# Performance work log

Hardware: AMD Instinct MI355X
Metric: run time of the kernel (lower is better)

The kernel has to match this reference:

```python
import jax, jax.numpy as jnp
import numpy as np

N_PROP, N_GRID, N_KEY, C_FEAT = 128, 216, 4096, 128
RADII = (0.8, 1.6)
NSAMPLES = (16, 16)
C_OUT = 64  # per-branch MLP output channels


def setup_inputs() -> dict:
    key = jax.random.key(0)
    ks = jax.random.split(key, 20)
    s = 0.05
    return {
        "wlh": jax.random.uniform(ks[0], (N_PROP, 3)) * 4.0 + 0.5,
        "center": jax.random.normal(ks[1], (N_PROP, 3)) * 5.0,
        "yaw": jax.random.uniform(ks[2], (N_PROP,)) * 2.0 * np.pi,
        "u": jax.random.uniform(ks[3], (N_PROP, N_GRID, 3)),
        "keypoints_xyz": jax.random.normal(ks[4], (1, N_KEY, 3)) * 5.0,
        "keypoints_features": jax.random.normal(ks[5], (1, C_FEAT, N_KEY)),
        "pn0_w1": jax.random.normal(ks[6], (C_OUT, C_FEAT + 3)) * s,
        "pn0_g1": jnp.ones((C_OUT,)), "pn0_b1": jnp.zeros((C_OUT,)),
        "pn0_w2": jax.random.normal(ks[7], (C_OUT, C_OUT)) * s,
        "pn0_g2": jnp.ones((C_OUT,)), "pn0_b2": jnp.zeros((C_OUT,)),
        "pn1_w1": jax.random.normal(ks[8], (C_OUT, C_FEAT + 3)) * s,
        "pn1_g1": jnp.ones((C_OUT,)), "pn1_b1": jnp.zeros((C_OUT,)),
        "pn1_w2": jax.random.normal(ks[9], (C_OUT, C_OUT)) * s,
        "pn1_g2": jnp.ones((C_OUT,)), "pn1_b2": jnp.zeros((C_OUT,)),
        "red_w1": jax.random.normal(ks[10], (256, N_GRID * 2 * C_OUT)) * 0.01,
        "red_b1": jnp.zeros((256,)),
        "red_w2": jax.random.normal(ks[11], (256, 256)) * s,
        "red_b2": jnp.zeros((256,)),
    }


def reference(wlh, center, yaw, u, keypoints_xyz, keypoints_features,
              pn0_w1, pn0_g1, pn0_b1, pn0_w2, pn0_g2, pn0_b2,
              pn1_w1, pn1_g1, pn1_b1, pn1_w2, pn1_g2, pn1_b2,
              red_w1, red_b1, red_w2, red_b2):
    n, m, _ = u.shape
    # --- sample gridpoints inside proposals and rotate by yaw around z ---
    gp = u * wlh[:, None, :]                                 # (n, m, 3)
    c, s = jnp.cos(yaw), jnp.sin(yaw)
    R = jnp.stack([c, -s, s, c], axis=-1).reshape(-1, 2, 2)   # (n, 2, 2)
    xy = jnp.einsum('njk,nmk->nmj', R, gp[..., :2])
    grid = jnp.concatenate([xy, gp[..., 2:]], -1) + center[:, None, :]
    grid = grid.reshape(-1, 3)                               # (G, 3), G = n*m

    kp = keypoints_xyz[0]                                    # (K, 3)
    kf = jnp.transpose(keypoints_features[0])                # (K, C)
    K = kp.shape[0]

    # squared distances (G, K) without materializing (G, K, 3)
    d2 = (jnp.sum(grid * grid, -1)[:, None]
          + jnp.sum(kp * kp, -1)[None, :]
          - 2.0 * grid @ kp.T)

    def ball_query(radius, nsample):
        # first `nsample` in-radius indices in original order; pad with first
        # hit; all-zeros if no point in radius (pointnet2 CUDA semantics).
        mask = d2 < radius * radius
        cand = jnp.where(mask, jnp.arange(K, dtype=jnp.int32), K)
        srt = jnp.sort(cand, axis=-1)[:, :nsample]           # (G, ns)
        first = srt[:, :1]
        return jnp.where(srt < K, srt, jnp.where(first < K, first, 0))

    def branch(radius, nsample, w1, g1, b1, w2, g2, b2):
        idx = ball_query(radius, nsample)                    # (G, ns)
        xyz = kp[idx] - grid[:, None, :]                     # (G, ns, 3)
        x = jnp.concatenate([xyz, kf[idx]], -1)              # (G, ns, 3+C)
        h = jax.nn.relu(jnp.einsum('gnc,oc->gno', x, w1) * g1 + b1)
        h = jax.nn.relu(jnp.einsum('gnc,oc->gno', h, w2) * g2 + b2)
        return jnp.max(h, axis=1)                            # (G, C_OUT)

    f0 = branch(RADII[0], NSAMPLES[0], pn0_w1, pn0_g1, pn0_b1, pn0_w2, pn0_g2, pn0_b2)
    f1 = branch(RADII[1], NSAMPLES[1], pn1_w1, pn1_g1, pn1_b1, pn1_w2, pn1_g2, pn1_b2)
    pooled = jnp.concatenate([f0, f1], -1)                   # (G, 2*C_OUT)
    Cp = pooled.shape[-1]

    # faithful replication of (1,C,n,m).permute(0,3,1,2).view(1,n,-1)
    t = pooled.reshape(n, m, Cp)                             # gridpoint order (n, m)
    red_in = jnp.transpose(t, (1, 2, 0)).reshape(1, n, m * Cp)

    h = jax.nn.relu(red_in @ red_w1.T + red_b1)
    return jax.nn.relu(h @ red_w2.T + red_b2)                # (1, n, 256)
```

## Files before the change

### kernel.cpp

```cpp
#include <hip/hip_runtime.h>
#include <hip/hip_bf16.h>

typedef unsigned short u16;
typedef unsigned int   u32;
typedef unsigned long long u64;

#define N_PROPC 128
#define N_GRIDC 216
#define G_TOT   27648
#define N_KEYC  4096
#define C_FEATC 128
#define R0SQ    0.64f
#define R1SQ    2.56f
#define BF16_ONES_DWORD 0x3F803F80u

typedef __attribute__((ext_vector_type(8))) short bf16x8;
typedef __attribute__((ext_vector_type(4))) float f32x4;

#if __has_builtin(__builtin_amdgcn_fcmpf)
#define BALLOT_LT(a, b) __builtin_amdgcn_fcmpf((a), (b), 4)
#else
#define BALLOT_LT(a, b) __ballot((a) < (b))
#endif

__device__ __forceinline__ float bf2f(u16 u) {
    return __uint_as_float(((u32)u) << 16);
}
__device__ __forceinline__ u16 f2bf(float f) {
    u32 u = __float_as_uint(f);
    u32 r = (u + 0x7fffu + ((u >> 16) & 1u)) >> 16;
    return (u16)r;
}
__device__ __forceinline__ bool is_bf16(const u32* flagp) {
    return *flagp == BF16_ONES_DWORD;
}
__device__ __forceinline__ float ld(const void* p, int i, bool bf) {
    return bf ? bf2f(((const u16*)p)[i]) : ((const float*)p)[i];
}
__device__ __forceinline__ u16 ldb(const void* p, int i, bool bf) {
    return bf ? ((const u16*)p)[i] : f2bf(((const float*)p)[i]);
}

__global__ __launch_bounds__(256) void prep_fused_kernel(
    const u32* __restrict__ flagp,
    const void* __restrict__ kxyz,
    const void* __restrict__ wlh, const void* __restrict__ center,
    const void* __restrict__ yaw, const void* __restrict__ uu,
    const void* __restrict__ kf,
    const void* __restrict__ w10, const void* __restrict__ g10, const void* __restrict__ b10,
    const void* __restrict__ w20, const void* __restrict__ g20, const void* __restrict__ b20,
    const void* __restrict__ w11, const void* __restrict__ g11, const void* __restrict__ b11,
    const void* __restrict__ w21, const void* __restrict__ g21, const void* __restrict__ b21,
    const void* __restrict__ rw2, const void* __restrict__ rw1,
    float4* __restrict__ kp4, float4* __restrict__ grid4, u16* __restrict__ kfT,
    u16* __restrict__ w1mf, u16* __restrict__ w2mf,
    float* __restrict__ g1f, float* __restrict__ b1f,
    float* __restrict__ g2f, float* __restrict__ b2f,
    float* __restrict__ w2rT, u16* __restrict__ rw1p)
{
    const bool bf = is_bf16(flagp);
    const int bid = blockIdx.x, tid = threadIdx.x;

    if (bid < 16) {
        int k = bid * 256 + tid;
        float x = ld(kxyz, k*3, bf), y = ld(kxyz, k*3+1, bf), z = ld(kxyz, k*3+2, bf);
        kp4[k] = make_float4(x, y, z, 0.0f);
    } else if (bid < 124) {
        int g = (bid - 16) * 256 + tid;
        int n = g / N_GRIDC;
        float ux = ld(uu, g*3, bf), uy = ld(uu, g*3+1, bf), uz = ld(uu, g*3+2, bf);
        float gpx = ux * ld(wlh, n*3, bf);
        float gpy = uy * ld(wlh, n*3+1, bf);
        float gpz = uz * ld(wlh, n*3+2, bf);
        float yv = ld(yaw, n, bf);
        float c = cosf(yv), sn = sinf(yv);
        float x = (c*gpx - sn*gpy) + ld(center, n*3, bf);
        float y = (sn*gpx + c*gpy) + ld(center, n*3+1, bf);
        float z = gpz + ld(center, n*3+2, bf);
        grid4[g] = make_float4(x, y, z, 0.0f);
    } else if (bid < 2172) {
        int t = (bid - 124) * 256 + tid;
        int key = t >> 7, feat = t & 127;
        kfT[t] = ldb(kf, feat * N_KEYC + key, bf);
    } else if (bid < 2174) {
        const int b = bid - 2172;
        const void* w1 = b ? w11 : w10; const void* g1v = b ? g11 : g10;
        const void* w2 = b ? w21 : w20; const void* g2v = b ? g21 : g20;
        const void* b1v = b ? b11 : b10; const void* b2v = b ? b21 : b20;
        for (int f = tid; f < 10240; f += 256) {
            int j = f & 7, t1 = f >> 3;
            int n = t1 & 15, t2 = t1 >> 4;
            int quad = t2 & 3, t3 = t2 >> 2;
            int kt = t3 % 5, nt = t3 / 5;
            int k = kt*32 + quad*8 + j;
            int o = nt*16 + n;
            u16 v = 0;
            if (k < 128)      v = ldb(w1, o*131 + 3 + k, bf);
            else if (k < 131) v = ldb(w1, o*131 + (k - 128), bf);
            w1mf[b*10240 + f] = v;
        }
        for (int f = tid; f < 4096; f += 256) {
            int j = f & 7, t1 = f >> 3;
            int n = t1 & 15, t2 = t1 >> 4;
            int quad = t2 & 3, t3 = t2 >> 2;
            int kt = t3 & 1, nt = t3 >> 1;
            int k = kt*32 + quad*8 + j;
            int o = nt*16 + n;
            w2mf[b*4096 + f] = ldb(w2, o*64 + k, bf);
        }
        if (tid < 64) {
            g1f[b*64 + tid] = ld(g1v, tid, bf);
            b1f[b*64 + tid] = ld(b1v, tid, bf);
            g2f[b*64 + tid] = ld(g2v, tid, bf);
            b2f[b*64 + tid] = ld(b2v, tid, bf);
        }
    } else if (bid < 2430) {
        int t = (bid - 2174) * 256 + tid;
        int o = t & 255, c = t >> 8;
        w2rT[c*256 + o] = ld(rw2, o*256 + c, bf);
    } else {
        int t = (bid - 2430) * 256 + tid;
        int j = t & 7;
        int n = (t >> 3) & 15;
        int quad = (t >> 7) & 3;
        int rest = t >> 9;
        int kk = rest % 864;
        int nt = rest / 864;
        int o = nt*16 + n;
        int k = kk*32 + quad*8 + j;
        rw1p[t] = ldb(rw1, o*27648 + k, bf);
    }
}

__global__ __launch_bounds__(256) void ballquery_kernel(
    const float4* __restrict__ kp4,
    const float4* __restrict__ grid4, u16* __restrict__ idx01)
{
    __shared__ __attribute__((aligned(16))) float4 sk[2048];
    const int tid = threadIdx.x;
    const int lane = tid & 63;
    const int g = blockIdx.x * 4 + (tid >> 6);
    const float4 gr = grid4[g];

    u64 mask0 = 0, mask1 = 0;
    #pragma unroll 1
    for (int pass = 0; pass < 2; ++pass) {
        if (pass) __syncthreads();
        for (int t = tid; t < 2048; t += 256) sk[t] = kp4[pass*2048 + t];
        __syncthreads();
        #pragma unroll
        for (int it = 0; it < 32; ++it) {
            const float4 kv = sk[it*64 + lane];
            const float dx = kv.x - gr.x;
            const float dy = kv.y - gr.y;
            const float dz = kv.z - gr.z;
            const float d = fmaf(dx, dx, fmaf(dy, dy, dz * dz));
            const u64 m1 = BALLOT_LT(d, R1SQ);
            const u64 m0 = BALLOT_LT(d, R0SQ);
            const int chunk = pass*32 + it;
            if (lane == chunk) { mask1 = m1; mask0 = m0; }
        }
    }

    u16* o0 = idx01 + (size_t)g * 16;
    u16* o1 = idx01 + (size_t)G_TOT * 16 + (size_t)g * 16;

    #pragma unroll
    for (int rad = 0; rad < 2; ++rad) {
        u64 mask = rad ? mask1 : mask0;
        u16* op = rad ? o1 : o0;
        const int cnt = __popcll(mask);
        int inc = cnt;
        #pragma unroll
        for (int d = 1; d < 64; d <<= 1) {
            int t = __shfl_up(inc, d);
            if (lane >= d) inc += t;
        }
        const int pre = inc - cnt;
        int firstk = (cnt > 0 && pre == 0) ? (lane*64 + __ffsll(mask) - 1) : 0x7FFFFFFF;
        #pragma unroll
        for (int d = 32; d >= 1; d >>= 1)
            firstk = min(firstk, __shfl_xor(firstk, d));
        const int total = __shfl(inc, 63);
        u64 mrem = mask;
        int p = pre;
        while (mrem != 0 && p < 16) {
            int j = __ffsll(mrem) - 1;
            op[p] = (u16)(lane*64 + j);
            mrem &= mrem - 1;
            ++p;
        }
        if (lane < 16 && lane >= total)
            op[lane] = (u16)(firstk == 0x7FFFFFFF ? 0 : firstk);
    }
}

__global__ __launch_bounds__(256) void pointnet_mfma_kernel(
    const float4* __restrict__ grid4, const float4* __restrict__ kp4,
    const u16* __restrict__ kfT,
    const u16* __restrict__ w1mf, const u16* __restrict__ w2mf,
    const float* __restrict__ g1f, const float* __restrict__ b1f,
    const float* __restrict__ g2f, const float* __restrict__ b2f,
    const u16* __restrict__ idx01, u16* __restrict__ ATb)
{
    __shared__ __attribute__((aligned(16))) u16 w1s[10240];
    __shared__ __attribute__((aligned(16))) u16 w2s[4096];
    __shared__ __attribute__((aligned(16))) u16 h1s[4][16*72];
    const int tid = threadIdx.x;
    const int branch = blockIdx.y;

    {
        const uint4* s1 = (const uint4*)(w1mf + branch*10240);
        uint4* d1 = (uint4*)w1s;
        for (int t = tid; t < 1280; t += 256) d1[t] = s1[t];
        const uint4* s2 = (const uint4*)(w2mf + branch*4096);
        uint4* d2 = (uint4*)w2s;
        for (int t = tid; t < 512; t += 256) d2[t] = s2[t];
    }
    __syncthreads();

    const int wid = tid >> 6, lane = tid & 63;
    const int n = lane & 15, quad = lane >> 4;
    const int g = blockIdx.x * 4 + wid;

    const int idx = idx01[(size_t)branch*(G_TOT*16) + g*16 + n] & (N_KEYC - 1);
    const float4 kp = kp4[idx];
    const float4 gr = grid4[g];

    bf16x8 axyz = (bf16x8)(short)0;
    if (quad == 0) {
        axyz[0] = (short)f2bf(kp.x - gr.x);
        axyz[1] = (short)f2bf(kp.y - gr.y);
        axyz[2] = (short)f2bf(kp.z - gr.z);
    }

    float g1v[4], b1v[4], g2v[4], b2v[4];
    #pragma unroll
    for (int nt = 0; nt < 4; ++nt) {
        g1v[nt] = g1f[branch*64 + nt*16 + n];
        b1v[nt] = b1f[branch*64 + nt*16 + n];
        g2v[nt] = g2f[branch*64 + nt*16 + n];
        b2v[nt] = b2f[branch*64 + nt*16 + n];
    }

    f32x4 acc0 = {0.f,0.f,0.f,0.f}, acc1 = acc0, acc2_ = acc0, acc3 = acc0;
    f32x4* acc[4] = {&acc0, &acc1, &acc2_, &acc3};

    const u16* __restrict__ arow = kfT + idx * C_FEATC;
    #pragma unroll
    for (int kt = 0; kt < 4; ++kt) {
        uint4 araw = *(const uint4*)(arow + kt*32 + quad*8);
        bf16x8 a;
        __builtin_memcpy(&a, &araw, 16);
        #pragma unroll
        for (int nt = 0; nt < 4; ++nt) {
            bf16x8 b = *(const bf16x8*)&w1s[(((nt*5 + kt)*4 + quad)*16 + n)*8];
            *acc[nt] = __builtin_amdgcn_mfma_f32_16x16x32_bf16(a, b, *acc[nt], 0, 0, 0);
        }
    }
    #pragma unroll
    for (int nt = 0; nt < 4; ++nt) {
        bf16x8 b = *(const bf16x8*)&w1s[(((nt*5 + 4)*4 + quad)*16 + n)*8];
        *acc[nt] = __builtin_amdgcn_mfma_f32_16x16x32_bf16(axyz, b, *acc[nt], 0, 0, 0);
    }

    u16* __restrict__ h1w = &h1s[wid][0];
    #pragma unroll
    for (int nt = 0; nt < 4; ++nt) {
        #pragma unroll
        for (int r = 0; r < 4; ++r) {
            float v = fmaxf(fmaf((*acc[nt])[r], g1v[nt], b1v[nt]), 0.0f);
            h1w[(quad*4 + r)*72 + nt*16 + n] = f2bf(v);
        }
    }

    f32x4 c0 = {0.f,0.f,0.f,0.f}, c1 = c0, c2 = c0, c3 = c0;
    f32x4* acc2[4] = {&c0, &c1, &c2, &c3};
    #pragma unroll
    for (int kt = 0; kt < 2; ++kt) {
        bf16x8 a2 = *(const bf16x8*)&h1w[n*72 + kt*32 + quad*8];
        #pragma unroll
        for (int nt = 0; nt < 4; ++nt) {
            bf16x8 b = *(const bf16x8*)&w2s[(((nt*2 + kt)*4 + quad)*16 + n)*8];
            *acc2[nt] = __builtin_amdgcn_mfma_f32_16x16x32_bf16(a2, b, *acc2[nt], 0, 0, 0);
        }
    }

    const int ni = g / N_GRIDC, mi = g % N_GRIDC;
    #pragma unroll
    for (int nt = 0; nt < 4; ++nt) {
        float v0 = fmaxf(fmaf((*acc2[nt])[0], g2v[nt], b2v[nt]), 0.0f);
        float v1 = fmaxf(fmaf((*acc2[nt])[1], g2v[nt], b2v[nt]), 0.0f);
        float v2 = fmaxf(fmaf((*acc2[nt])[2], g2v[nt], b2v[nt]), 0.0f);
        float v3 = fmaxf(fmaf((*acc2[nt])[3], g2v[nt], b2v[nt]), 0.0f);
        float v = fmaxf(fmaxf(v0, v1), fmaxf(v2, v3));
        v = fmaxf(v, __shfl_xor(v, 16));
        v = fmaxf(v, __shfl_xor(v, 32));
        if (lane < 16) {
            const int ci = branch*64 + nt*16 + n;
            const int flat = mi*16384 + ci*128 + ni;
            ATb[(size_t)(flat / 27648) * 27648 + (flat % 27648)] = f2bf(v);
        }
    }
}

__global__ __launch_bounds__(256) void red1_mfma_kernel(
    const u16* __restrict__ ATb, const u16* __restrict__ rw1p,
    float* __restrict__ part)
{
    const int tid = threadIdx.x;
    const int wid = tid >> 6, lane = tid & 63;
    const int w = blockIdx.x * 4 + wid;
    const int kc = w & 15;
    const int nt = (w >> 4) & 15;
    const int mt = w >> 8;
    const int n = lane & 15, quad = lane >> 4;

    const u16* __restrict__ arow = ATb + (size_t)(mt*16 + n) * 27648;
    const u16* __restrict__ bbase = rw1p + (((size_t)nt*864 + kc*54) * 4) * 16 * 8;

    f32x4 acc = {0.f, 0.f, 0.f, 0.f};
    #pragma unroll 2
    for (int s = 0; s < 54; ++s) {
        const int kk = kc*54 + s;
        uint4 araw = *(const uint4*)(arow + kk*32 + quad*8);
        bf16x8 a;
        __builtin_memcpy(&a, &araw, 16);
        bf16x8 b = *(const bf16x8*)(bbase + ((s*4 + quad)*16 + n)*8);
        acc = __builtin_amdgcn_mfma_f32_16x16x32_bf16(a, b, acc, 0, 0, 0);
    }
    #pragma unroll
    for (int r = 0; r < 4; ++r) {
        const int i = mt*16 + quad*4 + r;
        part[kc*32768 + i*256 + nt*16 + n] = acc[r];
    }
}

__global__ __launch_bounds__(256) void tail_kernel(
    const u32* __restrict__ flagp,
    const float* __restrict__ part, const void* __restrict__ rb1,
    const float* __restrict__ w2rT, const void* __restrict__ rb2,
    void* __restrict__ outp)
{
    __shared__ float hs[256];
    const bool bf = is_bf16(flagp);
    const int o = threadIdx.x, i = blockIdx.x;
    float s = ld(rb1, o, bf);
    #pragma unroll
    for (int kc = 0; kc < 16; ++kc) s += part[kc*32768 + i*256 + o];
    hs[o] = fmaxf(s, 0.0f);
    __syncthreads();
    float s2 = ld(rb2, o, bf);
    #pragma unroll 8
    for (int c = 0; c < 256; ++c)
        s2 = fmaf(hs[c], w2rT[c*256 + o], s2);
    float v = fmaxf(s2, 0.0f);
    if (bf) ((u16*)outp)[i*256 + o] = f2bf(v);
    else    ((float*)outp)[i*256 + o] = v;
}


extern "C" void kernel_launch(void* const* d_in, const int* in_sizes, int n_in,
                              void* d_out, int out_size, void* d_ws, size_t ws_size,
                              hipStream_t stream) {
    const void* wlh    = d_in[0];
    const void* center = d_in[1];
    const void* yaw    = d_in[2];
    const void* uu     = d_in[3];
    const void* kxyz   = d_in[4];
    const void* kfeat  = d_in[5];
    const void* p0w1 = d_in[6];  const void* p0g1 = d_in[7];
    const void* p0b1 = d_in[8];  const void* p0w2 = d_in[9];
    const void* p0g2 = d_in[10]; const void* p0b2 = d_in[11];
    const void* p1w1 = d_in[12]; const void* p1g1 = d_in[13];
    const void* p1b1 = d_in[14]; const void* p1w2 = d_in[15];
    const void* p1g2 = d_in[16]; const void* p1b2 = d_in[17];
    const void* rw1 = d_in[18];
    const void* rb1 = d_in[19];
    const void* rw2 = d_in[20];
    const void* rb2 = d_in[21];
    const u32* flagp = (const u32*)d_in[7];

    char* w = (char*)d_ws;
    float4* kp4   = (float4*)(w + 65536);
    float4* grid4 = (float4*)(w + 131072);
    u16*    kfT   = (u16*)(w + 573440);
    u16*    w1mf  = (u16*)(w + 1622016);
    u16*    w2mf  = (u16*)(w + 1662976);
    float*  g1f   = (float*)(w + 1679360);
    float*  b1f   = (float*)(w + 1679872);
    float*  g2f   = (float*)(w + 1680384);
    float*  b2f   = (float*)(w + 1680896);
    float*  w2rT  = (float*)(w + 1721856);
    u16*    idx01 = (u16*)(w + 1984000);
    u16*    ATb   = (u16*)(w + 3754496);
    u16*    rw1p  = (u16*)(w + 17910272);
    float*  part  = (float*)(w + 32066048);

    prep_fused_kernel<<<30078, 256, 0, stream>>>(flagp,
        kxyz, wlh, center, yaw, uu, kfeat,
        p0w1, p0g1, p0b1, p0w2, p0g2, p0b2,
        p1w1, p1g1, p1b1, p1w2, p1g2, p1b2,
        rw2, rw1,
        kp4, grid4, kfT,
        w1mf, w2mf, g1f, b1f, g2f, b2f, w2rT, rw1p);

    ballquery_kernel<<<G_TOT/4, 256, 0, stream>>>(kp4, grid4, idx01);

    dim3 pngrid(G_TOT/4, 2);
    pointnet_mfma_kernel<<<pngrid, 256, 0, stream>>>(grid4, kp4, kfT, w1mf, w2mf,
                                                     g1f, b1f, g2f, b2f, idx01, ATb);

    red1_mfma_kernel<<<512, 256, 0, stream>>>(ATb, rw1p, part);
    tail_kernel<<<128, 256, 0, stream>>>(flagp, part, rb1, w2rT, rb2, d_out);
}
```

Measured before the change: 290.2 us.

## Read red_w1 directly in GEMM and batch four gridpoints per wave

The pre-pass that repacked the large red_w1 matrix into an MFMA-friendly bf16 layout is removed. The reduction GEMM now loads rows of red_w1 directly and converts fp32 to bf16 on the fly, which avoids a full extra read and write of a 27648x256 matrix. Ball query and the PointNet kernel each process four gridpoints per wave, reusing the shared-memory keypoint loads and the staged weights across more work and cutting the block count. In exchange the GEMM B loads are strided by row instead of packed, and fp32 input doubles the bytes it reads for B.

```diff
diff --git a/kernel.cpp b/kernel.cpp
--- a/kernel.cpp
+++ b/kernel.cpp
@@ -51,12 +51,12 @@
     const void* __restrict__ w20, const void* __restrict__ g20, const void* __restrict__ b20,
     const void* __restrict__ w11, const void* __restrict__ g11, const void* __restrict__ b11,
     const void* __restrict__ w21, const void* __restrict__ g21, const void* __restrict__ b21,
-    const void* __restrict__ rw2, const void* __restrict__ rw1,
+    const void* __restrict__ rw2,
     float4* __restrict__ kp4, float4* __restrict__ grid4, u16* __restrict__ kfT,
     u16* __restrict__ w1mf, u16* __restrict__ w2mf,
     float* __restrict__ g1f, float* __restrict__ b1f,
     float* __restrict__ g2f, float* __restrict__ b2f,
-    float* __restrict__ w2rT, u16* __restrict__ rw1p)
+    float* __restrict__ w2rT)
 {
     const bool bf = is_bf16(flagp);
     const int bid = blockIdx.x, tid = threadIdx.x;
@@ -114,21 +114,10 @@
             g2f[b*64 + tid] = ld(g2v, tid, bf);
             b2f[b*64 + tid] = ld(b2v, tid, bf);
         }
-    } else if (bid < 2430) {
+    } else {
         int t = (bid - 2174) * 256 + tid;
         int o = t & 255, c = t >> 8;
         w2rT[c*256 + o] = ld(rw2, o*256 + c, bf);
-    } else {
-        int t = (bid - 2430) * 256 + tid;
-        int j = t & 7;
-        int n = (t >> 3) & 15;
-        int quad = (t >> 7) & 3;
-        int rest = t >> 9;
-        int kk = rest % 864;
-        int nt = rest / 864;
-        int o = nt*16 + n;
-        int k = kk*32 + quad*8 + j;
-        rw1p[t] = ldb(rw1, o*27648 + k, bf);
     }
 }
 
@@ -139,10 +128,15 @@
     __shared__ __attribute__((aligned(16))) float4 sk[2048];
     const int tid = threadIdx.x;
     const int lane = tid & 63;
-    const int g = blockIdx.x * 4 + (tid >> 6);
-    const float4 gr = grid4[g];
-
-    u64 mask0 = 0, mask1 = 0;
+    const int wid = tid >> 6;
+    const int g0 = blockIdx.x * 16 + wid * 4;
+    const float4 gra = grid4[g0];
+    const float4 grb = grid4[g0 + 1];
+    const float4 grc = grid4[g0 + 2];
+    const float4 grd = grid4[g0 + 3];
+
+    u64 m0[4] = {0, 0, 0, 0};
+    u64 m1[4] = {0, 0, 0, 0};
     #pragma unroll 1
     for (int pass = 0; pass < 2; ++pass) {
         if (pass) __syncthreads();
@@ -151,47 +145,62 @@
         #pragma unroll
         for (int it = 0; it < 32; ++it) {
             const float4 kv = sk[it*64 + lane];
-            const float dx = kv.x - gr.x;
-            const float dy = kv.y - gr.y;
-            const float dz = kv.z - gr.z;
-            const float d = fmaf(dx, dx, fmaf(dy, dy, dz * dz));
-            const u64 m1 = BALLOT_LT(d, R1SQ);
-            const u64 m0 = BALLOT_LT(d, R0SQ);
             const int chunk = pass*32 + it;
-            if (lane == chunk) { mask1 = m1; mask0 = m0; }
-        }
-    }
-
-    u16* o0 = idx01 + (size_t)g * 16;
-    u16* o1 = idx01 + (size_t)G_TOT * 16 + (size_t)g * 16;
+            float dx, dy, dz, d;
+            dx = kv.x - gra.x; dy = kv.y - gra.y; dz = kv.z - gra.z;
+            d = fmaf(dx, dx, fmaf(dy, dy, dz * dz));
+            const u64 a1 = BALLOT_LT(d, R1SQ); const u64 a0 = BALLOT_LT(d, R0SQ);
+            dx = kv.x - grb.x; dy = kv.y - grb.y; dz = kv.z - grb.z;
+            d = fmaf(dx, dx, fmaf(dy, dy, dz * dz));
+            const u64 b1m = BALLOT_LT(d, R1SQ); const u64 b0m = BALLOT_LT(d, R0SQ);
+            dx = kv.x - grc.x; dy = kv.y - grc.y; dz = kv.z - grc.z;
+            d = fmaf(dx, dx, fmaf(dy, dy, dz * dz));
+            const u64 c1m = BALLOT_LT(d, R1SQ); const u64 c0m = BALLOT_LT(d, R0SQ);
+            dx = kv.x - grd.x; dy = kv.y - grd.y; dz = kv.z - grd.z;
+            d = fmaf(dx, dx, fmaf(dy, dy, dz * dz));
+            const u64 d1m = BALLOT_LT(d, R1SQ); const u64 d0m = BALLOT_LT(d, R0SQ);
+            if (lane == chunk) {
+                m1[0] = a1; m0[0] = a0;
+                m1[1] = b1m; m0[1] = b0m;
+                m1[2] = c1m; m0[2] = c0m;
+                m1[3] = d1m; m0[3] = d0m;
+            }
+        }
+    }
 
     #pragma unroll
-    for (int rad = 0; rad < 2; ++rad) {
-        u64 mask = rad ? mask1 : mask0;
-        u16* op = rad ? o1 : o0;
-        const int cnt = __popcll(mask);
-        int inc = cnt;
-        #pragma unroll
-        for (int d = 1; d < 64; d <<= 1) {
-            int t = __shfl_up(inc, d);
-            if (lane >= d) inc += t;
-        }
-        const int pre = inc - cnt;
-        int firstk = (cnt > 0 && pre == 0) ? (lane*64 + __ffsll(mask) - 1) : 0x7FFFFFFF;
-        #pragma unroll
-        for (int d = 32; d >= 1; d >>= 1)
-            firstk = min(firstk, __shfl_xor(firstk, d));
-        const int total = __shfl(inc, 63);
-        u64 mrem = mask;
-        int p = pre;
-        while (mrem != 0 && p < 16) {
-            int j = __ffsll(mrem) - 1;
-            op[p] = (u16)(lane*64 + j);
-            mrem &= mrem - 1;
-            ++p;
-        }
-        if (lane < 16 && lane >= total)
-            op[lane] = (u16)(firstk == 0x7FFFFFFF ? 0 : firstk);
+    for (int gg = 0; gg < 4; ++gg) {
+        const int g = g0 + gg;
+        u16* o0 = idx01 + (size_t)g * 16;
+        u16* o1 = idx01 + (size_t)G_TOT * 16 + (size_t)g * 16;
+        #pragma unroll
+        for (int rad = 0; rad < 2; ++rad) {
+            u64 mask = rad ? m1[gg] : m0[gg];
+            u16* op = rad ? o1 : o0;
+            const int cnt = __popcll(mask);
+            int inc = cnt;
+            #pragma unroll
+            for (int d = 1; d < 64; d <<= 1) {
+                int t = __shfl_up(inc, d);
+                if (lane >= d) inc += t;
+            }
+            const int pre = inc - cnt;
+            int firstk = (cnt > 0 && pre == 0) ? (lane*64 + __ffsll(mask) - 1) : 0x7FFFFFFF;
+            #pragma unroll
+            for (int d = 32; d >= 1; d >>= 1)
+                firstk = min(firstk, __shfl_xor(firstk, d));
+            const int total = __shfl(inc, 63);
+            u64 mrem = mask;
+            int p = pre;
+            while (mrem != 0 && p < 16) {
+                int j = __ffsll(mrem) - 1;
+                op[p] = (u16)(lane*64 + j);
+                mrem &= mrem - 1;
+                ++p;
+            }
+            if (lane < 16 && lane >= total)
+                op[lane] = (u16)(firstk == 0x7FFFFFFF ? 0 : firstk);
+        }
     }
 }
 
@@ -221,18 +230,7 @@
 
     const int wid = tid >> 6, lane = tid & 63;
     const int n = lane & 15, quad = lane >> 4;
-    const int g = blockIdx.x * 4 + wid;
-
-    const int idx = idx01[(size_t)branch*(G_TOT*16) + g*16 + n] & (N_KEYC - 1);
-    const float4 kp = kp4[idx];
-    const float4 gr = grid4[g];
-
-    bf16x8 axyz = (bf16x8)(short)0;
-    if (quad == 0) {
-        axyz[0] = (short)f2bf(kp.x - gr.x);
-        axyz[1] = (short)f2bf(kp.y - gr.y);
-        axyz[2] = (short)f2bf(kp.z - gr.z);
-    }
+    const int gbase = blockIdx.x * 16 + wid * 4;
 
     float g1v[4], b1v[4], g2v[4], b2v[4];
     #pragma unroll
@@ -243,71 +241,89 @@
         b2v[nt] = b2f[branch*64 + nt*16 + n];
     }
 
-    f32x4 acc0 = {0.f,0.f,0.f,0.f}, acc1 = acc0, acc2_ = acc0, acc3 = acc0;
-    f32x4* acc[4] = {&acc0, &acc1, &acc2_, &acc3};
-
-    const u16* __restrict__ arow = kfT + idx * C_FEATC;
-    #pragma unroll
-    for (int kt = 0; kt < 4; ++kt) {
-        uint4 araw = *(const uint4*)(arow + kt*32 + quad*8);
-        bf16x8 a;
-        __builtin_memcpy(&a, &araw, 16);
+    u16* __restrict__ h1w = &h1s[wid][0];
+
+    #pragma unroll 1
+    for (int gg = 0; gg < 4; ++gg) {
+        const int g = gbase + gg;
+        const int idx = idx01[(size_t)branch*(G_TOT*16) + g*16 + n] & (N_KEYC - 1);
+        const float4 kp = kp4[idx];
+        const float4 gr = grid4[g];
+
+        bf16x8 axyz = (bf16x8)(short)0;
+        if (quad == 0) {
+            axyz[0] = (short)f2bf(kp.x - gr.x);
+            axyz[1] = (short)f2bf(kp.y - gr.y);
+            axyz[2] = (short)f2bf(kp.z - gr.z);
+        }
+
+        f32x4 acc0 = {0.f,0.f,0.f,0.f}, acc1 = acc0, acc2_ = acc0, acc3 = acc0;
+        f32x4* acc[4] = {&acc0, &acc1, &acc2_, &acc3};
+
+        const u16* __restrict__ arow = kfT + idx * C_FEATC;
+        #pragma unroll
+        for (int kt = 0; kt < 4; ++kt) {
+            uint4 araw = *(const uint4*)(arow + kt*32 + quad*8);
+            bf16x8 a;
+            __builtin_memcpy(&a, &araw, 16);
+            #pragma unroll
+            for (int nt = 0; nt < 4; ++nt) {
+                bf16x8 b = *(const bf16x8*)&w1s[(((nt*5 + kt)*4 + quad)*16 + n)*8];
+                *acc[nt] = __builtin_amdgcn_mfma_f32_16x16x32_bf16(a, b, *acc[nt], 0, 0, 0);
+            }
+        }
         #pragma unroll
         for (int nt = 0; nt < 4; ++nt) {
-            bf16x8 b = *(const bf16x8*)&w1s[(((nt*5 + kt)*4 + quad)*16 + n)*8];
-            *acc[nt] = __builtin_amdgcn_mfma_f32_16x16x32_bf16(a, b, *acc[nt], 0, 0, 0);
-        }
-    }
-    #pragma unroll
-    for (int nt = 0; nt < 4; ++nt) {
-        bf16x8 b = *(const bf16x8*)&w1s[(((nt*5 + 4)*4 + quad)*16 + n)*8];
-        *acc[nt] = __builtin_amdgcn_mfma_f32_16x16x32_bf16(axyz, b, *acc[nt], 0, 0, 0);
-    }
-
-    u16* __restrict__ h1w = &h1s[wid][0];
-    #pragma unroll
-    for (int nt = 0; nt < 4; ++nt) {
-        #pragma unroll
-        for (int r = 0; r < 4; ++r) {
-            float v = fmaxf(fmaf((*acc[nt])[r], g1v[nt], b1v[nt]), 0.0f);
-            h1w[(quad*4 + r)*72 + nt*16 + n] = f2bf(v);
-        }
-    }
-
-    f32x4 c0 = {0.f,0.f,0.f,0.f}, c1 = c0, c2 = c0, c3 = c0;
-    f32x4* acc2[4] = {&c0, &c1, &c2, &c3};
-    #pragma unroll
-    for (int kt = 0; kt < 2; ++kt) {
-        bf16x8 a2 = *(const bf16x8*)&h1w[n*72 + kt*32 + quad*8];
+            bf16x8 b = *(const bf16x8*)&w1s[(((nt*5 + 4)*4 + quad)*16 + n)*8];
+            *acc[nt] = __builtin_amdgcn_mfma_f32_16x16x32_bf16(axyz, b, *acc[nt], 0, 0, 0);
+        }
+
         #pragma unroll
         for (int nt = 0; nt < 4; ++nt) {
-            bf16x8 b = *(const bf16x8*)&w2s[(((nt*2 + kt)*4 + quad)*16 + n)*8];
-            *acc2[nt] = __builtin_amdgcn_mfma_f32_16x16x32_bf16(a2, b, *acc2[nt], 0, 0, 0);
-        }
-    }
-
-    const int ni = g / N_GRIDC, mi = g % N_GRIDC;
-    #pragma unroll
-    for (int nt = 0; nt < 4; ++nt) {
-        float v0 = fmaxf(fmaf((*acc2[nt])[0], g2v[nt], b2v[nt]), 0.0f);
-        float v1 = fmaxf(fmaf((*acc2[nt])[1], g2v[nt], b2v[nt]), 0.0f);
-        float v2 = fmaxf(fmaf((*acc2[nt])[2], g2v[nt], b2v[nt]), 0.0f);
-        float v3 = fmaxf(fmaf((*acc2[nt])[3], g2v[nt], b2v[nt]), 0.0f);
-        float v = fmaxf(fmaxf(v0, v1), fmaxf(v2, v3));
-        v = fmaxf(v, __shfl_xor(v, 16));
-        v = fmaxf(v, __shfl_xor(v, 32));
-        if (lane < 16) {
-            const int ci = branch*64 + nt*16 + n;
-            const int flat = mi*16384 + ci*128 + ni;
-            ATb[(size_t)(flat / 27648) * 27648 + (flat % 27648)] = f2bf(v);
+            #pragma unroll
+            for (int r = 0; r < 4; ++r) {
+                float v = fmaxf(fmaf((*acc[nt])[r], g1v[nt], b1v[nt]), 0.0f);
+                h1w[(quad*4 + r)*72 + nt*16 + n] = f2bf(v);
+            }
+        }
+
+        f32x4 c0 = {0.f,0.f,0.f,0.f}, c1 = c0, c2 = c0, c3 = c0;
+        f32x4* acc2[4] = {&c0, &c1, &c2, &c3};
+        #pragma unroll
+        for (int kt = 0; kt < 2; ++kt) {
+            bf16x8 a2 = *(const bf16x8*)&h1w[n*72 + kt*32 + quad*8];
+            #pragma unroll
+            for (int nt = 0; nt < 4; ++nt) {
+                bf16x8 b = *(const bf16x8*)&w2s[(((nt*2 + kt)*4 + quad)*16 + n)*8];
+                *acc2[nt] = __builtin_amdgcn_mfma_f32_16x16x32_bf16(a2, b, *acc2[nt], 0, 0, 0);
+            }
+        }
+
+        const int ni = g / N_GRIDC, mi = g % N_GRIDC;
+        #pragma unroll
+        for (int nt = 0; nt < 4; ++nt) {
+            float v0 = fmaxf(fmaf((*acc2[nt])[0], g2v[nt], b2v[nt]), 0.0f);
+            float v1 = fmaxf(fmaf((*acc2[nt])[1], g2v[nt], b2v[nt]), 0.0f);
+            float v2 = fmaxf(fmaf((*acc2[nt])[2], g2v[nt], b2v[nt]), 0.0f);
+            float v3 = fmaxf(fmaf((*acc2[nt])[3], g2v[nt], b2v[nt]), 0.0f);
+            float v = fmaxf(fmaxf(v0, v1), fmaxf(v2, v3));
+            v = fmaxf(v, __shfl_xor(v, 16));
+            v = fmaxf(v, __shfl_xor(v, 32));
+            if (lane < 16) {
+                const int ci = branch*64 + nt*16 + n;
+                const int flat = mi*16384 + ci*128 + ni;
+                ATb[(size_t)(flat / 27648) * 27648 + (flat % 27648)] = f2bf(v);
+            }
         }
     }
 }
 
 __global__ __launch_bounds__(256) void red1_mfma_kernel(
-    const u16* __restrict__ ATb, const u16* __restrict__ rw1p,
+    const u32* __restrict__ flagp,
+    const u16* __restrict__ ATb, const void* __restrict__ rw1,
     float* __restrict__ part)
 {
+    const bool bf = is_bf16(flagp);
     const int tid = threadIdx.x;
     const int wid = tid >> 6, lane = tid & 63;
     const int w = blockIdx.x * 4 + wid;
@@ -315,19 +331,41 @@
     const int nt = (w >> 4) & 15;
     const int mt = w >> 8;
     const int n = lane & 15, quad = lane >> 4;
+    const int o = nt*16 + n;
 
     const u16* __restrict__ arow = ATb + (size_t)(mt*16 + n) * 27648;
-    const u16* __restrict__ bbase = rw1p + (((size_t)nt*864 + kc*54) * 4) * 16 * 8;
 
     f32x4 acc = {0.f, 0.f, 0.f, 0.f};
-    #pragma unroll 2
-    for (int s = 0; s < 54; ++s) {
-        const int kk = kc*54 + s;
-        uint4 araw = *(const uint4*)(arow + kk*32 + quad*8);
-        bf16x8 a;
-        __builtin_memcpy(&a, &araw, 16);
-        bf16x8 b = *(const bf16x8*)(bbase + ((s*4 + quad)*16 + n)*8);
-        acc = __builtin_amdgcn_mfma_f32_16x16x32_bf16(a, b, acc, 0, 0, 0);
+    if (bf) {
+        const u16* __restrict__ brow = (const u16*)rw1 + (size_t)o * 27648;
+        #pragma unroll 2
+        for (int s = 0; s < 54; ++s) {
+            const int kk = kc*54 + s;
+            uint4 araw = *(const uint4*)(arow + kk*32 + quad*8);
+            bf16x8 a;
+            __builtin_memcpy(&a, &araw, 16);
+            uint4 braw = *(const uint4*)(brow + kk*32 + quad*8);
+            bf16x8 b;
+            __builtin_memcpy(&b, &braw, 16);
+            acc = __builtin_amdgcn_mfma_f32_16x16x32_bf16(a, b, acc, 0, 0, 0);
+        }
+    } else {
+        const float* __restrict__ brow = (const float*)rw1 + (size_t)o * 27648;
+        #pragma unroll 2
+        for (int s = 0; s < 54; ++s) {
+            const int kk = kc*54 + s;
+            uint4 araw = *(const uint4*)(arow + kk*32 + quad*8);
+            bf16x8 a;
+            __builtin_memcpy(&a, &araw, 16);
+            const float4 f0 = *(const float4*)(brow + kk*32 + quad*8);
+            const float4 f1 = *(const float4*)(brow + kk*32 + quad*8 + 4);
+            bf16x8 b;
+            b[0] = (short)f2bf(f0.x); b[1] = (short)f2bf(f0.y);
+            b[2] = (short)f2bf(f0.z); b[3] = (short)f2bf(f0.w);
+            b[4] = (short)f2bf(f1.x); b[5] = (short)f2bf(f1.y);
+            b[6] = (short)f2bf(f1.z); b[7] = (short)f2bf(f1.w);
+            acc = __builtin_amdgcn_mfma_f32_16x16x32_bf16(a, b, acc, 0, 0, 0);
+        }
     }
     #pragma unroll
     for (int r = 0; r < 4; ++r) {
@@ -394,23 +432,22 @@
     float*  w2rT  = (float*)(w + 1721856);
     u16*    idx01 = (u16*)(w + 1984000);
     u16*    ATb   = (u16*)(w + 3754496);
-    u16*    rw1p  = (u16*)(w + 17910272);
     float*  part  = (float*)(w + 32066048);
 
-    prep_fused_kernel<<<30078, 256, 0, stream>>>(flagp,
+    prep_fused_kernel<<<2430, 256, 0, stream>>>(flagp,
         kxyz, wlh, center, yaw, uu, kfeat,
         p0w1, p0g1, p0b1, p0w2, p0g2, p0b2,
         p1w1, p1g1, p1b1, p1w2, p1g2, p1b2,
-        rw2, rw1,
+        rw2,
         kp4, grid4, kfT,
-        w1mf, w2mf, g1f, b1f, g2f, b2f, w2rT, rw1p);
-
-    ballquery_kernel<<<G_TOT/4, 256, 0, stream>>>(kp4, grid4, idx01);
-
-    dim3 pngrid(G_TOT/4, 2);
+        w1mf, w2mf, g1f, b1f, g2f, b2f, w2rT);
+
+    ballquery_kernel<<<G_TOT/16, 256, 0, stream>>>(kp4, grid4, idx01);
+
+    dim3 pngrid(G_TOT/16, 2);
     pointnet_mfma_kernel<<<pngrid, 256, 0, stream>>>(grid4, kp4, kfT, w1mf, w2mf,
                                                      g1f, b1f, g2f, b2f, idx01, ATb);
 
-    red1_mfma_kernel<<<512, 256, 0, stream>>>(ATb, rw1p, part);
+    red1_mfma_kernel<<<512, 256, 0, stream>>>(flagp, ATb, rw1, part);
     tail_kernel<<<128, 256, 0, stream>>>(flagp, part, rb1, w2rT, rb2, d_out);
 }
```

Result: no change. 288.7 us (-0.5%).
